# Kernel tuning notes

Measured on AMD Instinct MI355X. Metric: run time of the kernel, lower is better.

The kernel has to match this reference:

```python
import jax, jax.numpy as jnp
import numpy as np

H = 8            # n_heads
CLIP = 10.0      # tanh_clipping
CAPACITY = 1.0   # AgentVRP.VEHICLE_CAPACITY


def setup_inputs() -> dict:
    key = jax.random.key(0)
    ks = jax.random.split(key, 12)
    B, N, D = 256, 1000, 128
    s = 1.0 / np.sqrt(D)  # keep pre-tanh logits in a sane range
    return {
        "embeddings": jax.random.normal(ks[0], (B, N, D), jnp.float32),
        "mean_graph_emb": jax.random.normal(ks[1], (B, D), jnp.float32),
        "used_capacity": jax.random.uniform(ks[2], (B, 1), jnp.float32),
        "prev_node": jax.random.randint(ks[3], (B, 1), 0, N),
        "mask": jax.random.randint(ks[4], (B, 1, N), 0, 2).astype(bool),
        "wq_context": jax.random.normal(ks[5], (D, D), jnp.float32) * s,
        "wq_step_context": jax.random.normal(ks[6], (D + 1, D), jnp.float32) * s,
        "wk": jax.random.normal(ks[7], (D, D), jnp.float32) * s,
        "wk_tanh": jax.random.normal(ks[8], (D, D), jnp.float32) * s,
        "wv": jax.random.normal(ks[9], (D, D), jnp.float32) * s,
        "w_out": jax.random.normal(ks[10], (D, D), jnp.float32) * s,
    }


def reference(embeddings, mean_graph_emb, used_capacity, prev_node, mask,
              wq_context, wq_step_context, wk, wk_tanh, wv, w_out):
    B, N, D = embeddings.shape
    hd = D // H
    neg_inf = jnp.float32(-np.inf)

    # --- get_projections ---
    K = (embeddings @ wk).reshape(B, N, H, hd).transpose(0, 2, 1, 3)       # bhnd
    V = (embeddings @ wv).reshape(B, N, H, hd).transpose(0, 2, 1, 3)       # bhnd
    K_tanh = embeddings @ wk_tanh                                          # bnD
    Q_context = (mean_graph_emb @ wq_context)[:, None, :]                  # b1D

    # --- get_step_context ---
    cur = jnp.take_along_axis(embeddings, prev_node[:, :, None].astype(jnp.int32), axis=1)  # b1D
    step_ctx = jnp.concatenate([cur, CAPACITY - used_capacity[:, :, None]], axis=-1)        # b1(D+1)
    Q = Q_context + step_ctx @ wq_step_context                             # b1D
    Qh = Q.reshape(B, 1, H, hd).transpose(0, 2, 1, 3)                      # bh1d

    # --- decoder_mha (seq_len_q = 1) ---
    compat = jnp.einsum('bhqd,bhnd->bhqn', Qh, K) / jnp.sqrt(jnp.float32(hd))
    compat = jnp.where(mask[:, None, :, :], neg_inf, compat)
    attn = jax.nn.softmax(compat, axis=-1)
    out = jnp.einsum('bhqn,bhnd->bhqd', attn, V)
    mha = out.transpose(0, 2, 1, 3).reshape(B, 1, D) @ w_out               # b1D

    # --- get_log_p (single head, tanh-clipped) ---
    logits = jnp.einsum('bqD,bnD->bqn', mha, K_tanh) / jnp.sqrt(jnp.float32(D))
    logits = jnp.tanh(logits) * CLIP
    logits = jnp.where(mask, neg_inf, logits)
    log_p = jax.nn.log_softmax(logits, axis=-1)                            # b1n
    return log_p
```

## Files before the change

### kernel.cpp

```cpp
#include <hip/hip_runtime.h>
#include <hip/hip_bf16.h>
#include <math.h>

constexpr int kB = 256;
constexpr int kN = 1000;
constexpr int kD = 128;
constexpr int kH = 8;

#define MASK_FILL (-1.0e30f)

__device__ __forceinline__ bool is_masked(const void* m, int flag, int idx) {
  if (flag == 1) return ((const unsigned char*)m)[idx] != 0;
  if (flag == 0) return ((const int*)m)[idx] != 0;
  return ((const float*)m)[idx] != 0.0f;
}

__global__ __launch_bounds__(1024, 4) void fused_all_kernel(
    const float* __restrict__ emb, const float* __restrict__ mge,
    const float* __restrict__ ucap, const int* __restrict__ prev,
    const float* __restrict__ wq_ctx, const float* __restrict__ wq_step,
    const float* __restrict__ wk, const void* __restrict__ mask,
    const float* __restrict__ wv_w, const float* __restrict__ w_out,
    const float* __restrict__ wk_tanh, float* __restrict__ out) {
  const int b = blockIdx.x, t = threadIdx.x;
  __shared__ __align__(16) float red[16][1024];
  __shared__ __align__(16) float qtl[8][132];
  __shared__ float curQ[kD];
  __shared__ float Qs[kD];
  __shared__ float mtl[kD];
  __shared__ float tl[kN];
  __shared__ float lred[16][8];
  __shared__ float linv8[8];
  __shared__ float sums[16];
  __shared__ unsigned char mloc[kN];
  __shared__ int nonbin_s, off_s;
  if (t == 0) { nonbin_s = 0; off_s = 0; }
  if (t < kD) curQ[t] = emb[((size_t)b * kN + prev[b]) * kD + t];
  {
    const unsigned char* mb = (const unsigned char*)mask;
    int ln = 0, lo = 0;
    for (int i = t; i < 4096; i += 1024) {
      const unsigned char v = mb[i];
      if (v > 1) ln = 1;
      if (v != 0 && (i & 3) != 0) lo = 1;
    }
    if (ln) atomicOr(&nonbin_s, 1);
    if (lo) atomicOr(&off_s, 1);
  }
  __syncthreads();
  const int flag = nonbin_s ? 2 : (off_s ? 1 : 0);
  for (int i = t; i < kN; i += 1024)
    mloc[i] = is_masked(mask, flag, b * kN + i) ? 1 : 0;
  {
    const int j = t >> 3, sgq = t & 7;
    float qacc = 0.f;
    const float* mger = mge + (size_t)b * kD;
    #pragma unroll
    for (int jj = 0; jj < 16; ++jj) {
      const int e = sgq * 16 + jj;
      qacc += mger[e] * wq_ctx[(size_t)e * kD + j]
            + curQ[e] * wq_step[(size_t)e * kD + j];
    }
    qacc += __shfl_xor(qacc, 1, 64);
    qacc += __shfl_xor(qacc, 2, 64);
    qacc += __shfl_xor(qacc, 4, 64);
    if (sgq == 0) Qs[j] = qacc + (1.0f - ucap[b]) * wq_step[(size_t)kD * kD + j];
  }
  __syncthreads();
  {
    const int h = t >> 7, d = t & 127;
    const float* wkr = wk + (size_t)d * kD + h * 16;
    const float* qsr = &Qs[h * 16];
    float a = 0.f;
    #pragma unroll
    for (int j = 0; j < 16; ++j) a += wkr[j] * qsr[j];
    qtl[h][d] = a * 0.25f;
  }
  __syncthreads();
  const int sg = t & 7, hg = (t >> 3) & 3, r8 = t >> 5;
  const float* qa = &qtl[hg * 2][sg * 16];
  const float* qb = &qtl[hg * 2 + 1][sg * 16];
  const float4 qA0 = *reinterpret_cast<const float4*>(qa);
  const float4 qA1 = *reinterpret_cast<const float4*>(qa + 4);
  const float4 qA2 = *reinterpret_cast<const float4*>(qa + 8);
  const float4 qA3 = *reinterpret_cast<const float4*>(qa + 12);
  const float4 qB0 = *reinterpret_cast<const float4*>(qb);
  const float4 qB1 = *reinterpret_cast<const float4*>(qb + 4);
  const float4 qB2 = *reinterpret_cast<const float4*>(qb + 8);
  const float4 qB3 = *reinterpret_cast<const float4*>(qb + 12);
  float4 aA0 = {}, aA1 = {}, aA2 = {}, aA3 = {};
  float4 aB0 = {}, aB1 = {}, aB2 = {}, aB3 = {};
  float lA = 0.f, lB = 0.f;
  const float* embb = emb + (size_t)b * kN * kD + sg * 16;
  for (int it = 0; it < 32; ++it) {
    const int n = it * 32 + r8;
    const bool valid = n < kN;
    const float* src = embb + (size_t)(valid ? n : 0) * kD;
    const float4 e0 = *reinterpret_cast<const float4*>(src);
    const float4 e1 = *reinterpret_cast<const float4*>(src + 4);
    const float4 e2 = *reinterpret_cast<const float4*>(src + 8);
    const float4 e3 = *reinterpret_cast<const float4*>(src + 12);
    float pA = e0.x*qA0.x + e0.y*qA0.y + e0.z*qA0.z + e0.w*qA0.w
             + e1.x*qA1.x + e1.y*qA1.y + e1.z*qA1.z + e1.w*qA1.w
             + e2.x*qA2.x + e2.y*qA2.y + e2.z*qA2.z + e2.w*qA2.w
             + e3.x*qA3.x + e3.y*qA3.y + e3.z*qA3.z + e3.w*qA3.w;
    float pB = e0.x*qB0.x + e0.y*qB0.y + e0.z*qB0.z + e0.w*qB0.w
             + e1.x*qB1.x + e1.y*qB1.y + e1.z*qB1.z + e1.w*qB1.w
             + e2.x*qB2.x + e2.y*qB2.y + e2.z*qB2.z + e2.w*qB2.w
             + e3.x*qB3.x + e3.y*qB3.y + e3.z*qB3.z + e3.w*qB3.w;
    pA += __shfl_xor(pA, 1, 64); pA += __shfl_xor(pA, 2, 64); pA += __shfl_xor(pA, 4, 64);
    pB += __shfl_xor(pB, 1, 64); pB += __shfl_xor(pB, 2, 64); pB += __shfl_xor(pB, 4, 64);
    const bool ok = valid && (mloc[valid ? n : 0] == 0);
    const float wA = ok ? __expf(pA) : 0.f;
    const float wB = ok ? __expf(pB) : 0.f;
    aA0.x += wA*e0.x; aA0.y += wA*e0.y; aA0.z += wA*e0.z; aA0.w += wA*e0.w;
    aA1.x += wA*e1.x; aA1.y += wA*e1.y; aA1.z += wA*e1.z; aA1.w += wA*e1.w;
    aA2.x += wA*e2.x; aA2.y += wA*e2.y; aA2.z += wA*e2.z; aA2.w += wA*e2.w;
    aA3.x += wA*e3.x; aA3.y += wA*e3.y; aA3.z += wA*e3.z; aA3.w += wA*e3.w;
    aB0.x += wB*e0.x; aB0.y += wB*e0.y; aB0.z += wB*e0.z; aB0.w += wB*e0.w;
    aB1.x += wB*e1.x; aB1.y += wB*e1.y; aB1.z += wB*e1.z; aB1.w += wB*e1.w;
    aB2.x += wB*e2.x; aB2.y += wB*e2.y; aB2.z += wB*e2.z; aB2.w += wB*e2.w;
    aB3.x += wB*e3.x; aB3.y += wB*e3.y; aB3.z += wB*e3.z; aB3.w += wB*e3.w;
    lA += wA; lB += wB;
  }
  #define M32(v) v.x += __shfl_xor(v.x,32,64); v.y += __shfl_xor(v.y,32,64); \
                 v.z += __shfl_xor(v.z,32,64); v.w += __shfl_xor(v.w,32,64);
  M32(aA0) M32(aA1) M32(aA2) M32(aA3) M32(aB0) M32(aB1) M32(aB2) M32(aB3)
  #undef M32
  lA += __shfl_xor(lA, 32, 64);
  lB += __shfl_xor(lB, 32, 64);
  const int w = t >> 6, wlane = t & 63;
  if (wlane < 32) {
    float* r0 = &red[w][(hg * 2) * kD + sg * 16];
    *reinterpret_cast<float4*>(r0)      = aA0;
    *reinterpret_cast<float4*>(r0 + 4)  = aA1;
    *reinterpret_cast<float4*>(r0 + 8)  = aA2;
    *reinterpret_cast<float4*>(r0 + 12) = aA3;
    float* r1 = &red[w][(hg * 2 + 1) * kD + sg * 16];
    *reinterpret_cast<float4*>(r1)      = aB0;
    *reinterpret_cast<float4*>(r1 + 4)  = aB1;
    *reinterpret_cast<float4*>(r1 + 8)  = aB2;
    *reinterpret_cast<float4*>(r1 + 12) = aB3;
    if (sg == 0) { lred[w][hg * 2] = lA; lred[w][hg * 2 + 1] = lB; }
  }
  __syncthreads();
  if (t < 8) {
    float l = 0.f;
    #pragma unroll
    for (int ww = 0; ww < 16; ++ww) l += lred[ww][t];
    linv8[t] = 1.0f / l;
  }
  __syncthreads();
  {
    float v = 0.f;
    #pragma unroll
    for (int ww = 0; ww < 16; ++ww) v += red[ww][t];
    qtl[t >> 7][t & 127] = v * linv8[t >> 7];
  }
  __syncthreads();
  const int j = t >> 3, sgq = t & 7;
  {
    const int h = j >> 4;
    float pp = 0.f;
    #pragma unroll
    for (int jj = 0; jj < 16; ++jj) {
      const int d = sgq * 16 + jj;
      pp += qtl[h][d] * wv_w[(size_t)d * kD + j];
    }
    pp += __shfl_xor(pp, 1, 64);
    pp += __shfl_xor(pp, 2, 64);
    pp += __shfl_xor(pp, 4, 64);
    if (sgq == 0) curQ[j] = pp;
  }
  __syncthreads();
  {
    float pp = 0.f;
    #pragma unroll
    for (int jj = 0; jj < 16; ++jj) {
      const int d = sgq * 16 + jj;
      pp += curQ[d] * w_out[(size_t)d * kD + j];
    }
    pp += __shfl_xor(pp, 1, 64);
    pp += __shfl_xor(pp, 2, 64);
    pp += __shfl_xor(pp, 4, 64);
    if (sgq == 0) Qs[j] = pp;
  }
  __syncthreads();
  {
    float pp = 0.f;
    const float* wr = wk_tanh + (size_t)j * kD + sgq * 16;
    #pragma unroll
    for (int jj = 0; jj < 16; ++jj)
      pp += wr[jj] * Qs[sgq * 16 + jj];
    pp += __shfl_xor(pp, 1, 64);
    pp += __shfl_xor(pp, 2, 64);
    pp += __shfl_xor(pp, 4, 64);
    if (sgq == 0) mtl[j] = pp * 0.08838834764831845f;
  }
  __syncthreads();
  const int seg = t & 7, rr8 = t >> 3;
  const float* mtb = &mtl[seg * 16];
  const float4 m0 = *reinterpret_cast<const float4*>(mtb);
  const float4 m1 = *reinterpret_cast<const float4*>(mtb + 4);
  const float4 m2 = *reinterpret_cast<const float4*>(mtb + 8);
  const float4 m3 = *reinterpret_cast<const float4*>(mtb + 12);
  float sumexp = 0.f;
  const float* embb2 = emb + (size_t)b * kN * kD;
  #pragma unroll
  for (int it = 0; it < 8; ++it) {
    const int n = it * 128 + rr8;
    const bool valid = n < kN;
    const int nc = valid ? n : kN - 1;
    const float* row = embb2 + (size_t)nc * kD + seg * 16;
    const float4 e0 = *reinterpret_cast<const float4*>(row);
    const float4 e1 = *reinterpret_cast<const float4*>(row + 4);
    const float4 e2 = *reinterpret_cast<const float4*>(row + 8);
    const float4 e3 = *reinterpret_cast<const float4*>(row + 12);
    float p = e0.x * m0.x + e0.y * m0.y + e0.z * m0.z + e0.w * m0.w
            + e1.x * m1.x + e1.y * m1.y + e1.z * m1.z + e1.w * m1.w
            + e2.x * m2.x + e2.y * m2.y + e2.z * m2.z + e2.w * m2.w
            + e3.x * m3.x + e3.y * m3.y + e3.z * m3.z + e3.w * m3.w;
    p += __shfl_xor(p, 1, 64);
    p += __shfl_xor(p, 2, 64);
    p += __shfl_xor(p, 4, 64);
    if (valid && seg == 0) {
      if (mloc[n]) {
        tl[n] = MASK_FILL;
      } else {
        const float tv = tanhf(p) * 10.0f;
        tl[n] = tv;
        sumexp += __expf(tv);
      }
    }
  }
  #pragma unroll
  for (int off = 1; off < 64; off <<= 1)
    sumexp += __shfl_xor(sumexp, off, 64);
  if ((t & 63) == 0) sums[t >> 6] = sumexp;
  __syncthreads();
  if (t < kN) {
    float total = 0.f;
    #pragma unroll
    for (int i = 0; i < 16; ++i) total += sums[i];
    const float lse = logf(total);
    const float v = tl[t];
    out[(size_t)b * kN + t] = (v == MASK_FILL) ? MASK_FILL : v - lse;
  }
}

extern "C" void kernel_launch(void* const* d_in, const int* in_sizes, int n_in,
                              void* d_out, int out_size, void* d_ws, size_t ws_size,
                              hipStream_t stream) {
  const float* emb     = (const float*)d_in[0];
  const float* mge     = (const float*)d_in[1];
  const float* ucap    = (const float*)d_in[2];
  const int*   prev    = (const int*)d_in[3];
  const void*  mask    = d_in[4];
  const float* wq_ctx  = (const float*)d_in[5];
  const float* wq_step = (const float*)d_in[6];
  const float* wk      = (const float*)d_in[7];
  const float* wk_tanh = (const float*)d_in[8];
  const float* wv_w    = (const float*)d_in[9];
  const float* w_out   = (const float*)d_in[10];
  float* out = (float*)d_out;

  hipLaunchKernelGGL(fused_all_kernel, dim3(kB), dim3(1024), 0, stream,
                     emb, mge, ucap, prev, wq_ctx, wq_step, wk, mask,
                     wv_w, w_out, wk_tanh, out);
}
```

Before: 77.19 us.

## Split attention pass across two blocks per batch and add second logits kernel

Splits the fused kernel in two. The first kernel runs two blocks per batch row, each covering 500 nodes of the attention accumulation, and writes partial weighted sums and softmax denominators to workspace. The second kernel merges the partials, applies the V, output and K_tanh projections, and computes the tanh-clipped log-softmax over all nodes. This doubles grid parallelism for the heavy attention pass on a 256-block launch, at the cost of an extra launch, workspace traffic, and recomputing the query projection in both split blocks.

```diff
diff --git a/kernel.cpp b/kernel.cpp
--- a/kernel.cpp
+++ b/kernel.cpp
@@ -15,25 +15,21 @@
   return ((const float*)m)[idx] != 0.0f;
 }
 
-__global__ __launch_bounds__(1024, 4) void fused_all_kernel(
+__global__ __launch_bounds__(1024) void attn_split_kernel(
     const float* __restrict__ emb, const float* __restrict__ mge,
     const float* __restrict__ ucap, const int* __restrict__ prev,
     const float* __restrict__ wq_ctx, const float* __restrict__ wq_step,
     const float* __restrict__ wk, const void* __restrict__ mask,
-    const float* __restrict__ wv_w, const float* __restrict__ w_out,
-    const float* __restrict__ wk_tanh, float* __restrict__ out) {
-  const int b = blockIdx.x, t = threadIdx.x;
+    float* __restrict__ pw, float* __restrict__ pl) {
+  const int s = blockIdx.x, b = blockIdx.y, t = threadIdx.x;
   __shared__ __align__(16) float red[16][1024];
   __shared__ __align__(16) float qtl[8][132];
   __shared__ float curQ[kD];
   __shared__ float Qs[kD];
-  __shared__ float mtl[kD];
-  __shared__ float tl[kN];
   __shared__ float lred[16][8];
-  __shared__ float linv8[8];
-  __shared__ float sums[16];
-  __shared__ unsigned char mloc[kN];
+  __shared__ unsigned char mloc[512];
   __shared__ int nonbin_s, off_s;
+  const int rowstart = s * 500, nrows = 500;
   if (t == 0) { nonbin_s = 0; off_s = 0; }
   if (t < kD) curQ[t] = emb[((size_t)b * kN + prev[b]) * kD + t];
   {
@@ -49,8 +45,8 @@
   }
   __syncthreads();
   const int flag = nonbin_s ? 2 : (off_s ? 1 : 0);
-  for (int i = t; i < kN; i += 1024)
-    mloc[i] = is_masked(mask, flag, b * kN + i) ? 1 : 0;
+  for (int i = t; i < nrows; i += 1024)
+    mloc[i] = is_masked(mask, flag, b * kN + rowstart + i) ? 1 : 0;
   {
     const int j = t >> 3, sgq = t & 7;
     float qacc = 0.f;
@@ -91,11 +87,11 @@
   float4 aA0 = {}, aA1 = {}, aA2 = {}, aA3 = {};
   float4 aB0 = {}, aB1 = {}, aB2 = {}, aB3 = {};
   float lA = 0.f, lB = 0.f;
-  const float* embb = emb + (size_t)b * kN * kD + sg * 16;
-  for (int it = 0; it < 32; ++it) {
-    const int n = it * 32 + r8;
-    const bool valid = n < kN;
-    const float* src = embb + (size_t)(valid ? n : 0) * kD;
+  const float* embb = emb + ((size_t)b * kN + rowstart) * kD + sg * 16;
+  for (int it = 0; it < 16; ++it) {
+    const int lr = it * 32 + r8;
+    const bool valid = lr < nrows;
+    const float* src = embb + (size_t)(valid ? lr : 0) * kD;
     const float4 e0 = *reinterpret_cast<const float4*>(src);
     const float4 e1 = *reinterpret_cast<const float4*>(src + 4);
     const float4 e2 = *reinterpret_cast<const float4*>(src + 8);
@@ -110,7 +106,7 @@
              + e3.x*qB3.x + e3.y*qB3.y + e3.z*qB3.z + e3.w*qB3.w;
     pA += __shfl_xor(pA, 1, 64); pA += __shfl_xor(pA, 2, 64); pA += __shfl_xor(pA, 4, 64);
     pB += __shfl_xor(pB, 1, 64); pB += __shfl_xor(pB, 2, 64); pB += __shfl_xor(pB, 4, 64);
-    const bool ok = valid && (mloc[valid ? n : 0] == 0);
+    const bool ok = valid && (mloc[valid ? lr : 0] == 0);
     const float wA = ok ? __expf(pA) : 0.f;
     const float wB = ok ? __expf(pB) : 0.f;
     aA0.x += wA*e0.x; aA0.y += wA*e0.y; aA0.z += wA*e0.z; aA0.w += wA*e0.w;
@@ -144,74 +140,116 @@
     if (sg == 0) { lred[w][hg * 2] = lA; lred[w][hg * 2 + 1] = lB; }
   }
   __syncthreads();
+  {
+    float v = 0.f;
+    #pragma unroll
+    for (int ww = 0; ww < 16; ++ww) v += red[ww][t];
+    pw[(size_t)(b * 2 + s) * 1024 + t] = v;
+  }
   if (t < 8) {
     float l = 0.f;
     #pragma unroll
     for (int ww = 0; ww < 16; ++ww) l += lred[ww][t];
-    linv8[t] = 1.0f / l;
-  }
-  __syncthreads();
-  {
+    pl[(size_t)(b * 2 + s) * kH + t] = l;
+  }
+}
+
+__global__ __launch_bounds__(1024) void logits_all_kernel(
+    const float* __restrict__ emb, const void* __restrict__ mask,
+    const float* __restrict__ pw, const float* __restrict__ pl,
+    const float* __restrict__ wv_w, const float* __restrict__ w_out,
+    const float* __restrict__ wk_tanh, float* __restrict__ out, int nsplit) {
+  const int b = blockIdx.x, t = threadIdx.x;
+  __shared__ float wsuml[8][132];
+  __shared__ float outflat[128];
+  __shared__ float mhal[128];
+  __shared__ float mtl[128];
+  __shared__ float linv[8];
+  __shared__ float tl[kN];
+  __shared__ float sums[16];
+  __shared__ int nonbin_s, off_s;
+  if (t == 0) { nonbin_s = 0; off_s = 0; }
+  if (t < 8) {
+    float l = 0.f;
+    for (int s2 = 0; s2 < nsplit; ++s2)
+      l += pl[(size_t)(b * nsplit + s2) * kH + t];
+    linv[t] = 1.0f / l;
+  }
+  __syncthreads();
+  {
+    const unsigned char* mb = (const unsigned char*)mask;
+    int ln = 0, lo = 0;
+    for (int i = t; i < 4096; i += 1024) {
+      const unsigned char v = mb[i];
+      if (v > 1) ln = 1;
+      if (v != 0 && (i & 3) != 0) lo = 1;
+    }
+    if (ln) atomicOr(&nonbin_s, 1);
+    if (lo) atomicOr(&off_s, 1);
+  }
+  {
+    const int h = t >> 7, d = t & 127;
     float v = 0.f;
-    #pragma unroll
-    for (int ww = 0; ww < 16; ++ww) v += red[ww][t];
-    qtl[t >> 7][t & 127] = v * linv8[t >> 7];
-  }
-  __syncthreads();
-  const int j = t >> 3, sgq = t & 7;
+    for (int s2 = 0; s2 < nsplit; ++s2)
+      v += pw[(size_t)(b * nsplit + s2) * 1024 + t];
+    wsuml[h][d] = v * linv[h];
+  }
+  __syncthreads();
+  const int flag = nonbin_s ? 2 : (off_s ? 1 : 0);
+  const int j = t >> 3, sg = t & 7;
   {
     const int h = j >> 4;
     float pp = 0.f;
     #pragma unroll
     for (int jj = 0; jj < 16; ++jj) {
-      const int d = sgq * 16 + jj;
-      pp += qtl[h][d] * wv_w[(size_t)d * kD + j];
+      const int d = sg * 16 + jj;
+      pp += wsuml[h][d] * wv_w[(size_t)d * kD + j];
     }
     pp += __shfl_xor(pp, 1, 64);
     pp += __shfl_xor(pp, 2, 64);
     pp += __shfl_xor(pp, 4, 64);
-    if (sgq == 0) curQ[j] = pp;
+    if (sg == 0) outflat[j] = pp;
   }
   __syncthreads();
   {
     float pp = 0.f;
     #pragma unroll
     for (int jj = 0; jj < 16; ++jj) {
-      const int d = sgq * 16 + jj;
-      pp += curQ[d] * w_out[(size_t)d * kD + j];
+      const int d = sg * 16 + jj;
+      pp += outflat[d] * w_out[(size_t)d * kD + j];
     }
     pp += __shfl_xor(pp, 1, 64);
     pp += __shfl_xor(pp, 2, 64);
     pp += __shfl_xor(pp, 4, 64);
-    if (sgq == 0) Qs[j] = pp;
+    if (sg == 0) mhal[j] = pp;
   }
   __syncthreads();
   {
     float pp = 0.f;
-    const float* wr = wk_tanh + (size_t)j * kD + sgq * 16;
+    const float* wr = wk_tanh + (size_t)j * kD + sg * 16;
     #pragma unroll
     for (int jj = 0; jj < 16; ++jj)
-      pp += wr[jj] * Qs[sgq * 16 + jj];
+      pp += wr[jj] * mhal[sg * 16 + jj];
     pp += __shfl_xor(pp, 1, 64);
     pp += __shfl_xor(pp, 2, 64);
     pp += __shfl_xor(pp, 4, 64);
-    if (sgq == 0) mtl[j] = pp * 0.08838834764831845f;
-  }
-  __syncthreads();
-  const int seg = t & 7, rr8 = t >> 3;
+    if (sg == 0) mtl[j] = pp * 0.08838834764831845f;
+  }
+  __syncthreads();
+  const int seg = t & 7, r8 = t >> 3;
   const float* mtb = &mtl[seg * 16];
   const float4 m0 = *reinterpret_cast<const float4*>(mtb);
   const float4 m1 = *reinterpret_cast<const float4*>(mtb + 4);
   const float4 m2 = *reinterpret_cast<const float4*>(mtb + 8);
   const float4 m3 = *reinterpret_cast<const float4*>(mtb + 12);
   float sumexp = 0.f;
-  const float* embb2 = emb + (size_t)b * kN * kD;
+  const float* embb = emb + (size_t)b * kN * kD;
   #pragma unroll
   for (int it = 0; it < 8; ++it) {
-    const int n = it * 128 + rr8;
+    const int n = it * 128 + r8;
     const bool valid = n < kN;
     const int nc = valid ? n : kN - 1;
-    const float* row = embb2 + (size_t)nc * kD + seg * 16;
+    const float* row = embb + (size_t)nc * kD + seg * 16;
     const float4 e0 = *reinterpret_cast<const float4*>(row);
     const float4 e1 = *reinterpret_cast<const float4*>(row + 4);
     const float4 e2 = *reinterpret_cast<const float4*>(row + 8);
@@ -224,7 +262,7 @@
     p += __shfl_xor(p, 2, 64);
     p += __shfl_xor(p, 4, 64);
     if (valid && seg == 0) {
-      if (mloc[n]) {
+      if (is_masked(mask, flag, b * kN + n)) {
         tl[n] = MASK_FILL;
       } else {
         const float tv = tanhf(p) * 10.0f;
@@ -264,7 +302,11 @@
   const float* w_out   = (const float*)d_in[10];
   float* out = (float*)d_out;
 
-  hipLaunchKernelGGL(fused_all_kernel, dim3(kB), dim3(1024), 0, stream,
-                     emb, mge, ucap, prev, wq_ctx, wq_step, wk, mask,
-                     wv_w, w_out, wk_tanh, out);
+  float* pw = (float*)((char*)d_ws + 256);
+  float* pl = (float*)((char*)d_ws + 256 + (size_t)kB * 2 * 1024 * 4);
+
+  hipLaunchKernelGGL(attn_split_kernel, dim3(2, kB), dim3(1024), 0, stream,
+                     emb, mge, ucap, prev, wq_ctx, wq_step, wk, mask, pw, pl);
+  hipLaunchKernelGGL(logits_all_kernel, dim3(kB), dim3(1024), 0, stream,
+                     emb, mask, pw, pl, wv_w, w_out, wk_tanh, out, 2);
 }
```

New measurement: 95.56 us. 1.24x slower.
